# Performance work log

Measured on AMD Instinct MI355X. Metric: run time of the kernel, lower is better.

The kernel has to match this reference:

```python
import jax, jax.numpy as jnp
import numpy as np

L = 4096            # lattice side (L_num)
R = 4.8             # public-goods enhancement factor r
GAMMA = 0.8         # discount
EPSILON = 0.02      # exploration rate
ETA = 0.8           # Q-learning mixing rate (self.eta)
NEG_BIG = 1.0e9


def neigh5(x):
    # 3x3 cross kernel conv on wrap-padded grid == circular 5-point sum
    return (x + jnp.roll(x, 1, 0) + jnp.roll(x, -1, 0)
              + jnp.roll(x, 1, 1) + jnp.roll(x, -1, 1))


def setup_inputs() -> dict:
    key = jax.random.key(0)
    k1, k2, k3, k4, k5 = jax.random.split(key, 5)
    N = L * L
    type_t_matrix = jax.random.randint(k1, (L, L), 0, 2, dtype=jnp.int32)
    # q_table ~ 0.5*randn + [2.0, 1.5] offset on next-state axis (as in __init__)
    offs = jnp.array([2.0, 1.5], dtype=jnp.float32)
    q_table = jax.random.normal(k2, (N, 2, 2), dtype=jnp.float32) * 0.5 + offs[None, None, :]
    rand_tensor = jax.random.uniform(k3, (N, 2), dtype=jnp.float32)
    random_type = jax.random.randint(k4, (L, L), 0, 2, dtype=jnp.int32)
    epsilon_rand = jax.random.uniform(k5, (L, L), dtype=jnp.float32)
    return {"type_t_matrix": type_t_matrix, "q_table": q_table,
            "rand_tensor": rand_tensor, "random_type": random_type,
            "epsilon_rand": epsilon_rand}


def reference(type_t_matrix, q_table, rand_tensor, random_type, epsilon_rand):
    N = L * L
    # --- calculation_value: profit on toroidal lattice ---
    c = (type_t_matrix == 1).astype(jnp.float32)  # cooperators
    d = (type_t_matrix == 0).astype(jnp.float32)  # defectors
    coop_num = neigh5(c)                          # cooperators in 5-neighborhood
    c_profit = coop_num / 5.0 * R - 1.0
    d_profit = coop_num / 5.0 * R
    profit = neigh5(c_profit) * c + neigh5(d_profit) * d  # (L, L)

    # --- type_matrix_change: epsilon-greedy action selection ---
    A = type_t_matrix.reshape(-1)                 # current state per cell (N,)
    C = jnp.arange(N)
    Qp = q_table[C, A]                            # (N, 2) action values
    maxv = jnp.max(Qp, axis=1, keepdims=True)
    max_t = (Qp == maxv).astype(jnp.float32)      # argmax mask (ties)
    masked = max_t - (1.0 - max_t) * NEG_BIG
    greedy = jnp.argmax(masked + rand_tensor, axis=1)  # random tie-break
    explore_mask = (epsilon_rand >= EPSILON).reshape(-1)
    B = jnp.where(explore_mask, greedy.astype(jnp.int32), random_type.reshape(-1))

    # --- updateQMatrix: indexed gather/scatter Q update ---
    max_values = jnp.max(q_table[C, B], axis=1)   # max_a' Q[s', a']
    upd = (1.0 - ETA) * q_table[C, A, B] + ETA * (profit.reshape(-1) + GAMMA * max_values)
    q_new = q_table.at[C, A, B].set(upd)

    type_t1_matrix = B.reshape(L, L).astype(jnp.float32)
    return type_t1_matrix, q_new, profit
```

## Files before the change

### kernel.cpp

```cpp
#include <hip/hip_runtime.h>

#define L 4096
#define LMASK 4095
#define NCELL (L * L)
#define TILE 64
#define HALO 2
#define SDIM (TILE + 2 * HALO)

typedef float f32x2 __attribute__((ext_vector_type(2)));

__global__ __launch_bounds__(256) void spgg_qlearn_kernel(
    const int*    __restrict__ type_t,
    const float4* __restrict__ qtab,
    const float*  __restrict__ rnd,
    const int*    __restrict__ rtype,
    const float*  __restrict__ eps,
    float*        __restrict__ out_type,
    float4*       __restrict__ out_q,
    float*        __restrict__ out_profit)
{
    __shared__ int s_t[SDIM * SDIM];

    const int tx = threadIdx.x;
    const int ty = threadIdx.y;
    const int tid = ty * 64 + tx;
    const int tileR0 = blockIdx.y * TILE;
    const int tileC0 = blockIdx.x * TILE;

    for (int idx = tid; idx < SDIM * SDIM; idx += 256) {
        const int ly = idx / SDIM;
        const int lx = idx - ly * SDIM;
        const int gr = (tileR0 + ly - HALO) & LMASK;
        const int gc = (tileC0 + lx - HALO) & LMASK;
        s_t[idx] = type_t[gr * L + gc];
    }
    __syncthreads();

    const int gc = tileC0 + tx;
    const int sc = tx + HALO;

    #pragma unroll 4
    for (int k = 0; k < 16; ++k) {
        const int r = k * 4 + ty;
        const int gr = tileR0 + r;
        const int i = gr * L + gc;

        float4 q = qtab[i];
        const float e = eps[i];
        const int rt = rtype[i];

        const int sr = r + HALO;
        const int t00 = s_t[sr * SDIM + sc];
        const int cross = s_t[(sr - 1) * SDIM + sc] + s_t[(sr + 1) * SDIM + sc]
                        + s_t[sr * SDIM + sc - 1]   + s_t[sr * SDIM + sc + 1];
        const int diag  = s_t[(sr - 1) * SDIM + sc - 1] + s_t[(sr - 1) * SDIM + sc + 1]
                        + s_t[(sr + 1) * SDIM + sc - 1] + s_t[(sr + 1) * SDIM + sc + 1];
        const int far   = s_t[(sr - 2) * SDIM + sc] + s_t[(sr + 2) * SDIM + sc]
                        + s_t[sr * SDIM + sc - 2]   + s_t[sr * SDIM + sc + 2];
        const int w13 = 5 * t00 + 2 * cross + 2 * diag + far;

        const float profit = 0.96f * (float)w13 - 5.0f * (float)t00;

        const int A = t00;
        const float qa0 = A ? q.z : q.x;
        const float qa1 = A ? q.w : q.y;

        int greedy = (qa1 > qa0) ? 1 : 0;

        if (__any(qa0 == qa1)) {
            f32x2 rv;
            asm volatile("global_load_dwordx2 %0, %1, off\n\t"
                         "s_waitcnt vmcnt(0)"
                         : "=v"(rv) : "v"(rnd + 2 * (long)i));
            if (qa0 == qa1) greedy = (rv.y > rv.x) ? 1 : 0;
        }

        const int B = (e >= 0.02f) ? greedy : rt;

        const float qb0 = B ? q.z : q.x;
        const float qb1 = B ? q.w : q.y;
        const float maxv = fmaxf(qb0, qb1);

        const int ab = A * 2 + B;
        const float qab = (ab == 0) ? q.x : (ab == 1) ? q.y : (ab == 2) ? q.z : q.w;
        const float upd = 0.2f * qab + 0.8f * (profit + 0.8f * maxv);

        q.x = (ab == 0) ? upd : q.x;
        q.y = (ab == 1) ? upd : q.y;
        q.z = (ab == 2) ? upd : q.z;
        q.w = (ab == 3) ? upd : q.w;

        out_type[i]   = (float)B;
        out_q[i]      = q;
        out_profit[i] = profit;
    }
}

extern "C" void kernel_launch(void* const* d_in, const int* in_sizes, int n_in,
                              void* d_out, int out_size, void* d_ws, size_t ws_size,
                              hipStream_t stream) {
    const int*    type_t = (const int*)d_in[0];
    const float4* qtab   = (const float4*)d_in[1];
    const float*  rnd    = (const float*)d_in[2];
    const int*    rtype  = (const int*)d_in[3];
    const float*  eps    = (const float*)d_in[4];

    float* out    = (float*)d_out;
    float* o_type = out;
    float4* o_q   = (float4*)(out + NCELL);
    float* o_prof = out + 5 * (size_t)NCELL;

    dim3 block(64, 4);
    dim3 grid(L / TILE, L / TILE);
    spgg_qlearn_kernel<<<grid, block, 0, stream>>>(
        type_t, qtab, rnd, rtype, eps, o_type, o_q, o_prof);
}
```

Baseline: 174.7 us.

## Replace shared-memory halo tiling with direct cached global stencil loads

```diff
diff --git a/kernel.cpp b/kernel.cpp
--- a/kernel.cpp
+++ b/kernel.cpp
@@ -3,9 +3,6 @@
 #define L 4096
 #define LMASK 4095
 #define NCELL (L * L)
-#define TILE 64
-#define HALO 2
-#define SDIM (TILE + 2 * HALO)
 
 typedef float f32x2 __attribute__((ext_vector_type(2)));
 
@@ -19,81 +16,75 @@
     float4*       __restrict__ out_q,
     float*        __restrict__ out_profit)
 {
-    __shared__ int s_t[SDIM * SDIM];
+    const int i = blockIdx.x * 256 + threadIdx.x;
+    const int r = i >> 12;
+    const int c = i & LMASK;
 
-    const int tx = threadIdx.x;
-    const int ty = threadIdx.y;
-    const int tid = ty * 64 + tx;
-    const int tileR0 = blockIdx.y * TILE;
-    const int tileC0 = blockIdx.x * TILE;
+    const int r0  = r << 12;
+    const int rm1 = ((r - 1) & LMASK) << 12;
+    const int rp1 = ((r + 1) & LMASK) << 12;
+    const int rm2 = ((r - 2) & LMASK) << 12;
+    const int rp2 = ((r + 2) & LMASK) << 12;
+    const int cm1 = (c - 1) & LMASK;
+    const int cp1 = (c + 1) & LMASK;
+    const int cm2 = (c - 2) & LMASK;
+    const int cp2 = (c + 2) & LMASK;
 
-    for (int idx = tid; idx < SDIM * SDIM; idx += 256) {
-        const int ly = idx / SDIM;
-        const int lx = idx - ly * SDIM;
-        const int gr = (tileR0 + ly - HALO) & LMASK;
-        const int gc = (tileC0 + lx - HALO) & LMASK;
-        s_t[idx] = type_t[gr * L + gc];
+    const int t00 = type_t[r0 + c];
+    const int f1  = type_t[rm2 + c];
+    const int f2  = type_t[rp2 + c];
+    const int f3  = type_t[r0 + cm2];
+    const int f4  = type_t[r0 + cp2];
+    const int x1  = type_t[rm1 + c];
+    const int x2  = type_t[rp1 + c];
+    const int x3  = type_t[r0 + cm1];
+    const int x4  = type_t[r0 + cp1];
+    const int g1  = type_t[rm1 + cm1];
+    const int g2  = type_t[rm1 + cp1];
+    const int g3  = type_t[rp1 + cm1];
+    const int g4  = type_t[rp1 + cp1];
+
+    float4 q = qtab[i];
+    const float e = eps[i];
+    const int  rt = rtype[i];
+
+    const int w13 = 5 * t00 + 2 * (x1 + x2 + x3 + x4) + 2 * (g1 + g2 + g3 + g4)
+                  + (f1 + f2 + f3 + f4);
+
+    const float profit = 0.96f * (float)w13 - 5.0f * (float)t00;
+
+    const int A = t00;
+    const float qa0 = A ? q.z : q.x;
+    const float qa1 = A ? q.w : q.y;
+
+    int greedy = (qa1 > qa0) ? 1 : 0;
+
+    if (__any(qa0 == qa1)) {
+        f32x2 rv;
+        asm volatile("global_load_dwordx2 %0, %1, off\n\t"
+                     "s_waitcnt vmcnt(0)"
+                     : "=v"(rv) : "v"(rnd + 2 * (long)i));
+        if (qa0 == qa1) greedy = (rv.y > rv.x) ? 1 : 0;
     }
-    __syncthreads();
 
-    const int gc = tileC0 + tx;
-    const int sc = tx + HALO;
+    const int B = (e >= 0.02f) ? greedy : rt;
 
-    #pragma unroll 4
-    for (int k = 0; k < 16; ++k) {
-        const int r = k * 4 + ty;
-        const int gr = tileR0 + r;
-        const int i = gr * L + gc;
+    const float qb0 = B ? q.z : q.x;
+    const float qb1 = B ? q.w : q.y;
+    const float maxv = fmaxf(qb0, qb1);
 
-        float4 q = qtab[i];
-        const float e = eps[i];
-        const int rt = rtype[i];
+    const int ab = A * 2 + B;
+    const float qab = (ab == 0) ? q.x : (ab == 1) ? q.y : (ab == 2) ? q.z : q.w;
+    const float upd = 0.2f * qab + 0.8f * (profit + 0.8f * maxv);
 
-        const int sr = r + HALO;
-        const int t00 = s_t[sr * SDIM + sc];
-        const int cross = s_t[(sr - 1) * SDIM + sc] + s_t[(sr + 1) * SDIM + sc]
-                        + s_t[sr * SDIM + sc - 1]   + s_t[sr * SDIM + sc + 1];
-        const int diag  = s_t[(sr - 1) * SDIM + sc - 1] + s_t[(sr - 1) * SDIM + sc + 1]
-                        + s_t[(sr + 1) * SDIM + sc - 1] + s_t[(sr + 1) * SDIM + sc + 1];
-        const int far   = s_t[(sr - 2) * SDIM + sc] + s_t[(sr + 2) * SDIM + sc]
-                        + s_t[sr * SDIM + sc - 2]   + s_t[sr * SDIM + sc + 2];
-        const int w13 = 5 * t00 + 2 * cross + 2 * diag + far;
+    q.x = (ab == 0) ? upd : q.x;
+    q.y = (ab == 1) ? upd : q.y;
+    q.z = (ab == 2) ? upd : q.z;
+    q.w = (ab == 3) ? upd : q.w;
 
-        const float profit = 0.96f * (float)w13 - 5.0f * (float)t00;
-
-        const int A = t00;
-        const float qa0 = A ? q.z : q.x;
-        const float qa1 = A ? q.w : q.y;
-
-        int greedy = (qa1 > qa0) ? 1 : 0;
-
-        if (__any(qa0 == qa1)) {
-            f32x2 rv;
-            asm volatile("global_load_dwordx2 %0, %1, off\n\t"
-                         "s_waitcnt vmcnt(0)"
-                         : "=v"(rv) : "v"(rnd + 2 * (long)i));
-            if (qa0 == qa1) greedy = (rv.y > rv.x) ? 1 : 0;
-        }
-
-        const int B = (e >= 0.02f) ? greedy : rt;
-
-        const float qb0 = B ? q.z : q.x;
-        const float qb1 = B ? q.w : q.y;
-        const float maxv = fmaxf(qb0, qb1);
-
-        const int ab = A * 2 + B;
-        const float qab = (ab == 0) ? q.x : (ab == 1) ? q.y : (ab == 2) ? q.z : q.w;
-        const float upd = 0.2f * qab + 0.8f * (profit + 0.8f * maxv);
-
-        q.x = (ab == 0) ? upd : q.x;
-        q.y = (ab == 1) ? upd : q.y;
-        q.z = (ab == 2) ? upd : q.z;
-        q.w = (ab == 3) ? upd : q.w;
-
-        out_type[i]   = (float)B;
-        out_q[i]      = q;
-        out_profit[i] = profit;
-    }
+    out_type[i]   = (float)B;
+    out_q[i]      = q;
+    out_profit[i] = profit;
 }
 
 extern "C" void kernel_launch(void* const* d_in, const int* in_sizes, int n_in,
@@ -110,8 +101,6 @@
     float4* o_q   = (float4*)(out + NCELL);
     float* o_prof = out + 5 * (size_t)NCELL;
 
-    dim3 block(64, 4);
-    dim3 grid(L / TILE, L / TILE);
-    spgg_qlearn_kernel<<<grid, block, 0, stream>>>(
+    spgg_qlearn_kernel<<<NCELL / 256, 256, 0, stream>>>(
         type_t, qtab, rnd, rtype, eps, o_type, o_q, o_prof);
 }
```

Measured after the change: 160.7 us. 1.09x faster.
